# Optimization experiments

Hardware: AMD Instinct MI355X
Metric: run time of the kernel (lower is better)

Reference implementation:

```python
import jax, jax.numpy as jnp
import numpy as np

H = 1024          # hidden_size
NH = 16           # num_heads
NKV = 16          # num_kv_heads
HD = 64           # head_dim
INTER = 2048      # intermediate_size
E = 8             # num_experts
TOPK = 2
EPS = 1e-6


def setup_inputs() -> dict:
    key = jax.random.key(0)
    ks = jax.random.split(key, 8)
    B, S = 4, 1024
    total_qkv = (NH + 2 * NKV) * HD
    return {
        "hidden_states": jax.random.normal(ks[0], (B, S, H), dtype=jnp.float32),
        "attention_mask": jnp.zeros((1, 1, S, S), dtype=jnp.float32),
        "input_layernorm": jnp.ones((H,), dtype=jnp.float32),
        "post_attention_layernorm": jnp.ones((H,), dtype=jnp.float32),
        "qkv_w": jax.random.normal(ks[1], (H, total_qkv), dtype=jnp.float32) * 0.02,
        "o_w": jax.random.normal(ks[2], (NH * HD, H), dtype=jnp.float32) * 0.02,
        "router_w": jax.random.normal(ks[3], (H, E), dtype=jnp.float32) * 0.02,
        "gate_up_proj": jax.random.normal(ks[4], (E, H, 2 * INTER), dtype=jnp.float32) * 0.02,
        "down_proj": jax.random.normal(ks[5], (E, INTER, H), dtype=jnp.float32) * 0.02,
    }


def _rmsnorm(x, w):
    var = jnp.mean(x * x, axis=-1, keepdims=True)
    return x * jax.lax.rsqrt(var + EPS) * w


def _attention_block(x, attention_mask, input_layernorm, qkv_w, o_w):
    B, S, _ = x.shape
    h = _rmsnorm(x, input_layernorm)
    qkv = h @ qkv_w  # [B,S,(NH+2*NKV)*HD]
    tq, tkv = NH * HD, NKV * HD
    q = qkv[..., :tq].reshape(B, S, NH, HD).transpose(0, 2, 1, 3)
    k = qkv[..., tq:tq + tkv].reshape(B, S, NKV, HD).transpose(0, 2, 1, 3)
    v = qkv[..., tq + tkv:].reshape(B, S, NKV, HD).transpose(0, 2, 1, 3)
    scores = jnp.einsum('bhqd,bhkd->bhqk', q, k) / np.sqrt(HD).astype(np.float32)
    scores = scores + attention_mask
    attn = jax.nn.softmax(scores, axis=-1)
    out = jnp.einsum('bhqk,bhkd->bhqd', attn, v)
    out = out.transpose(0, 2, 1, 3).reshape(B, S, NH * HD)
    return out @ o_w


def _moe_block(x, post_attention_layernorm, router_w, gate_up_proj, down_proj):
    B, S, _ = x.shape
    xf = x.reshape(-1, H)                      # [T,H]
    T = xf.shape[0]
    hf = _rmsnorm(xf, post_attention_layernorm)
    logits = hf @ router_w                     # [T,E]
    probs = jax.nn.softmax(logits, axis=-1)
    w, idx = jax.lax.top_k(probs, TOPK)        # [T,TOPK]
    w = w / jnp.sum(w, axis=-1, keepdims=True)
    # combine weights scattered into dense [T,E] (0 for unrouted experts)
    cw = jnp.zeros((T, E), dtype=hf.dtype).at[jnp.arange(T)[:, None], idx].add(w)
    out = jnp.zeros_like(hf)
    for e in range(E):  # fixed small expert loop, fully vectorized over tokens
        gu = hf @ gate_up_proj[e]              # [T,2*INTER]
        g, u = gu[:, :INTER], gu[:, INTER:]
        act = jax.nn.silu(g) * u
        out = out + cw[:, e:e + 1] * (act @ down_proj[e])
    return out.reshape(B, S, H)


def reference(hidden_states, attention_mask, input_layernorm, post_attention_layernorm,
              qkv_w, o_w, router_w, gate_up_proj, down_proj):
    x = hidden_states
    x = x + _attention_block(x, attention_mask, input_layernorm, qkv_w, o_w)
    x = x + _moe_block(x, post_attention_layernorm, router_w, gate_up_proj, down_proj)
    return x
```

## Files before the change

kernel.cpp:

```cpp
#include <hip/hip_runtime.h>
#include <cstdint>
#include <cmath>

#define T_TOK 4096
#define H_DIM 1024
#define QKV_N 3072
#define S_LEN 1024
#define INTER_DIM 2048
#define MAXROWS 9216

typedef unsigned short u16;
using f32x4 = __attribute__((ext_vector_type(4))) float;
using h16x8 = __attribute__((ext_vector_type(8))) _Float16;
using h16x4 = __attribute__((ext_vector_type(4))) _Float16;
using i32x4 = __attribute__((ext_vector_type(4))) int;
using u16x4 = __attribute__((ext_vector_type(4))) u16;
using u16x8 = __attribute__((ext_vector_type(8))) u16;

__device__ __forceinline__ float bf2f(u16 u){ return __uint_as_float(((uint32_t)u)<<16); }
__device__ __forceinline__ u16 f2bf(float f){
  uint32_t x = __float_as_uint(f);
  uint32_t r = x + 0x7FFFu + ((x>>16)&1u);
  return (u16)(r>>16);
}
__device__ __forceinline__ f32x4 mfma16(h16x8 a, h16x8 b, f32x4 c){
  return __builtin_amdgcn_mfma_f32_16x16x32_f16(a,b,c,0,0,0);
}
__device__ __forceinline__ float rsqrt_acc(float v){
  float r = rsqrtf(v);
  r = r*(1.5f - 0.5f*v*r*r);
  r = r*(1.5f - 0.5f*v*r*r);
  return r;
}
__device__ __forceinline__ float ldin(const void* p, size_t i, int is32){
  return is32 ? ((const float*)p)[i] : bf2f(((const u16*)p)[i]);
}
__device__ __forceinline__ int kslot_sw(int k, int noct){
  return (k&7) | (((k>>3) ^ (noct&3))<<3);
}
__device__ __forceinline__ void gll16(const void* g, void* l){
  __builtin_amdgcn_global_load_lds(
      (const __attribute__((address_space(1))) void*)g,
      (__attribute__((address_space(3))) void*)l, 16, 0, 0);
}

__global__ void k_detect(const uint32_t* __restrict__ x, int* __restrict__ dflag){
  uint32_t u = x[threadIdx.x];
  int e = (u>>23)&0xFF;
  int ok = (e>=103 && e<=150);
  unsigned long long m = __ballot(ok);
  if (threadIdx.x==0) *dflag = (__popcll(m) >= 48) ? 1 : 0;
}

__global__ __launch_bounds__(256) void k_trans2(const void* __restrict__ src,
    _Float16* __restrict__ dst, int R, int C, const int* __restrict__ df){
  const int is32 = *df;
  __shared__ _Float16 t[64][65];
  size_t bo = (size_t)blockIdx.z * R * C;
  int c0 = blockIdx.x<<6, r0 = blockIdx.y<<6;
  int ty = threadIdx.x>>3, tx = threadIdx.x&7;
  #pragma unroll
  for (int rr=0; rr<2; rr++){
    int r = rr*32 + ty;
    size_t gi = bo + (size_t)(r0+r)*C + c0 + tx*8;
    _Float16 v[8];
    if (is32){
      f32x4 a0 = *(const f32x4*)&((const float*)src)[gi];
      f32x4 a1 = *(const f32x4*)&((const float*)src)[gi+4];
      #pragma unroll
      for (int i=0;i<4;i++){ v[i]=(_Float16)a0[i]; v[4+i]=(_Float16)a1[i]; }
    } else {
      u16x8 a = *(const u16x8*)&((const u16*)src)[gi];
      #pragma unroll
      for (int i=0;i<8;i++) v[i]=(_Float16)bf2f(a[i]);
    }
    #pragma unroll
    for (int i=0;i<8;i++) t[r][tx*8+i] = v[i];
  }
  __syncthreads();
  #pragma unroll
  for (int rr=0; rr<2; rr++){
    int n = rr*32 + ty;
    h16x8 v;
    #pragma unroll
    for (int i=0;i<8;i++) v[i] = t[tx*8+i][n];
    *(h16x8*)&dst[bo + (size_t)(c0+n)*R + r0 + tx*8] = v;
  }
}

__global__ __launch_bounds__(256) void k_maskchk(const void* __restrict__ m, int* __restrict__ flag,
                                                 const int* __restrict__ df){
  const int is32 = *df;
  int i = (blockIdx.x*256 + threadIdx.x)*4;
  int nz = 0;
  if (is32){
    f32x4 v = *(const f32x4*)&((const float*)m)[i];
    nz = (v[0]!=0.f)||(v[1]!=0.f)||(v[2]!=0.f)||(v[3]!=0.f);
  } else {
    u16x4 v = *(const u16x4*)&((const u16*)m)[i];
    nz = ((v[0]|v[1]|v[2]|v[3]) & 0x7FFF) != 0;
  }
  if (nz) atomicOr(flag, 1);
}

__global__ __launch_bounds__(256) void k_rms1(const void* __restrict__ x, const void* __restrict__ w,
                                              _Float16* __restrict__ hhi, _Float16* __restrict__ hlo,
                                              const int* __restrict__ df){
  const int is32 = *df;
  int t = blockIdx.x, tid = threadIdx.x;
  size_t base = (size_t)t*H_DIM + tid*4;
  float f[4];
  #pragma unroll
  for (int m=0;m<4;m++) f[m] = ldin(x, base+m, is32);
  float ss = f[0]*f[0] + f[1]*f[1] + f[2]*f[2] + f[3]*f[3];
  #pragma unroll
  for (int off=32; off>0; off>>=1) ss += __shfl_down(ss, off, 64);
  __shared__ float red[4];
  if ((tid & 63) == 0) red[tid>>6] = ss;
  __syncthreads();
  float rstd = rsqrt_acc((red[0]+red[1]+red[2]+red[3]) * (1.0f/H_DIM) + 1e-6f);
  h16x4 oh, ol;
  #pragma unroll
  for (int m=0;m<4;m++){
    float v = f[m]*rstd*ldin(w, tid*4+m, is32);
    _Float16 hh = (_Float16)v;
    oh[m] = hh;
    ol[m] = (_Float16)(v - (float)hh);
  }
  *(h16x4*)&hhi[base] = oh;
  *(h16x4*)&hlo[base] = ol;
}

template<int EPI>
__global__ __launch_bounds__(256) void k_gemm_hl(const _Float16* __restrict__ Ah,
    const _Float16* __restrict__ Al, const _Float16* __restrict__ Bt,
    float* __restrict__ C, _Float16* __restrict__ Chi, _Float16* __restrict__ Clo,
    const void* __restrict__ res, int N, int K, const int* __restrict__ df){
  const int is32 = (EPI==1) ? *df : 0;
  __shared__ __align__(16) _Float16 AhS[128*32];
  __shared__ __align__(16) _Float16 AlS[128*32];
  __shared__ __align__(16) _Float16 Bs[128*32];
  int tid = threadIdx.x, lane = tid&63, wvx = tid>>6;
  int wr = wvx>>1, wc = wvx&1, quad = lane>>4, lrow = lane&15;
  int m0 = blockIdx.y<<7, n0 = blockIdx.x<<7;
  int ar = tid>>2, acg = (tid&3)*8;
  const _Float16* a0h = &Ah[(size_t)(m0+ar)*K + acg];
  const _Float16* a1h = &Ah[(size_t)(m0+64+ar)*K + acg];
  const _Float16* a0l = &Al[(size_t)(m0+ar)*K + acg];
  const _Float16* a1l = &Al[(size_t)(m0+64+ar)*K + acg];
  const _Float16* b0  = &Bt[(size_t)(n0+ar)*K + acg];
  const _Float16* b1  = &Bt[(size_t)(n0+64+ar)*K + acg];
  f32x4 acc[4][4] = {};
  for (int k0=0; k0<K; k0+=32){
    gll16(a0h + k0, &AhS[wvx*512]);
    gll16(a1h + k0, &AhS[2048 + wvx*512]);
    gll16(a0l + k0, &AlS[wvx*512]);
    gll16(a1l + k0, &AlS[2048 + wvx*512]);
    gll16(b0  + k0, &Bs[wvx*512]);
    gll16(b1  + k0, &Bs[2048 + wvx*512]);
    __syncthreads();
    h16x8 ah[4], al[4], bb[4];
    #pragma unroll
    for (int i=0;i<4;i++){
      ah[i] = *(const h16x8*)&AhS[(wr*64 + i*16 + lrow)*32 + quad*8];
      al[i] = *(const h16x8*)&AlS[(wr*64 + i*16 + lrow)*32 + quad*8];
    }
    #pragma unroll
    for (int j=0;j<4;j++) bb[j] = *(const h16x8*)&Bs[(wc*64 + j*16 + lrow)*32 + quad*8];
    #pragma unroll
    for (int i=0;i<4;i++)
      #pragma unroll
      for (int j=0;j<4;j++){
        acc[i][j] = mfma16(ah[i], bb[j], acc[i][j]);
        acc[i][j] = mfma16(al[i], bb[j], acc[i][j]);
      }
    __syncthreads();
  }
  #pragma unroll
  for (int i=0;i<4;i++)
    #pragma unroll
    for (int j=0;j<4;j++){
      int col = n0 + wc*64 + j*16 + lrow;
      #pragma unroll
      for (int r=0;r<4;r++){
        int row = m0 + wr*64 + i*16 + quad*4 + r;
        size_t idx = (size_t)row*N + col;
        float v = acc[i][j][r];
        if (EPI==1){
          v += ldin(res, idx, is32);
          C[idx] = v;
        } else {
          _Float16 hh = (_Float16)v;
          Chi[idx] = hh;
          Clo[idx] = (_Float16)(v - (float)hh);
        }
      }
    }
}

__global__ __launch_bounds__(256) void k_vt(const _Float16* __restrict__ qh,
    const _Float16* __restrict__ ql, _Float16* __restrict__ vth, _Float16* __restrict__ vtl){
  __shared__ _Float16 th[64][72];
  __shared__ _Float16 tl[64][72];
  int bh = blockIdx.y;
  int b = bh>>4, h = bh&15;
  int key0 = blockIdx.x<<6;
  size_t tok0 = (size_t)b*S_LEN;
  int ty = threadIdx.x>>3, tx = threadIdx.x&7;
  #pragma unroll
  for (int rr=0; rr<2; rr++){
    int r = rr*32 + ty;
    size_t gi = (tok0 + key0 + r)*(size_t)QKV_N + 2048 + h*64 + tx*8;
    h16x8 vh_ = *(const h16x8*)&qh[gi];
    h16x8 vl_ = *(const h16x8*)&ql[gi];
    #pragma unroll
    for (int i=0;i<8;i++){ th[r][tx*8+i] = vh_[i]; tl[r][tx*8+i] = vl_[i]; }
  }
  __syncthreads();
  size_t dbase = (size_t)bh*64*1024;
  #pragma unroll
  for (int rr=0; rr<2; rr++){
    int d = rr*32 + ty;
    h16x8 oh, ol;
    #pragma unroll
    for (int i=0;i<8;i++){ oh[i] = th[tx*8+i][d]; ol[i] = tl[tx*8+i][d]; }
    *(h16x8*)&vth[dbase + (size_t)d*1024 + key0 + tx*8] = oh;
    *(h16x8*)&vtl[dbase + (size_t)d*1024 + key0 + tx*8] = ol;
  }
}

__global__ __launch_bounds__(256, 2) void k_attn(const _Float16* __restrict__ qkvh,
    const _Float16* __restrict__ qkvl, const _Float16* __restrict__ vth_g,
    const _Float16* __restrict__ vtl_g, const void* __restrict__ mask,
    const int* __restrict__ mflag, _Float16* __restrict__ ohi, _Float16* __restrict__ olo,
    const int* __restrict__ df){
  const int is32 = *df;
  __shared__ __align__(16) _Float16 pool[32768];
  _Float16* Khi = pool;
  _Float16* Klo = pool + 4096;
  _Float16* Vth = pool + 8192;
  _Float16* Vtl = pool + 12288;
  _Float16* Phi = pool + 16384;
  _Float16* Plo = pool + 24576;
  int qt = blockIdx.x, bh = blockIdx.y;
  int b = bh>>4, h = bh&15;
  int tid = threadIdx.x, lane = tid&63, wvx = tid>>6, quad = lane>>4, lrow = lane&15;
  size_t tok0 = (size_t)b*S_LEN;
  int q0 = qt<<7;
  {
    int r = tid>>2, cg = (tid&3)*8;
    #pragma unroll
    for (int p=0;p<2;p++)
      #pragma unroll
      for (int g=0;g<2;g++){
        size_t src = (tok0 + q0 + g*64 + r)*(size_t)QKV_N + h*64 + p*32 + cg;
        gll16(&qkvh[src], &pool[p*4096 + g*2048 + wvx*512]);
        gll16(&qkvl[src], &pool[8192 + p*4096 + g*2048 + wvx*512]);
      }
  }
  __syncthreads();
  h16x8 qfh[2][2], qfl[2][2];
  #pragma unroll
  for (int p=0;p<2;p++)
    #pragma unroll
    for (int i=0;i<2;i++){
      qfh[p][i] = *(const h16x8*)&pool[(p*128 + wvx*32 + i*16 + lrow)*32 + quad*8];
      qfl[p][i] = *(const h16x8*)&pool[8192 + (p*128 + wvx*32 + i*16 + lrow)*32 + quad*8];
    }
  int useMask = *mflag;
  float mrun[2][4], lrun[2][4];
  f32x4 oacc[2][4] = {};
  #pragma unroll
  for (int i=0;i<2;i++)
    #pragma unroll
    for (int r=0;r<4;r++){ mrun[i][r] = -INFINITY; lrun[i][r] = 0.f; }
  size_t vbase = (size_t)bh*64*1024;
  int krow = tid>>3;
  int c8   = (tid&7)*8;
  int rsw  = ((tid>>3)&7)<<3;
  int fsw  = (lrow&7)<<3;
  size_t ksrc0 = (tok0 + krow)*(size_t)QKV_N + 1024 + h*64 + c8;
  size_t vsrc0 = vbase + (size_t)krow*1024 + c8;
  h16x8 kh_r[2], kl_r[2], vh_r[2], vl_r[2];
  {
    size_t ks0 = ksrc0, ks1 = ksrc0 + (size_t)32*QKV_N;
    kh_r[0] = *(const h16x8*)&qkvh[ks0];  kl_r[0] = *(const h16x8*)&qkvl[ks0];
    kh_r[1] = *(const h16x8*)&qkvh[ks1];  kl_r[1] = *(const h16x8*)&qkvl[ks1];
    size_t vs0 = vsrc0, vs1 = vsrc0 + 32*1024;
    vh_r[0] = *(const h16x8*)&vth_g[vs0]; vl_r[0] = *(const h16x8*)&vtl_g[vs0];
    vh_r[1] = *(const h16x8*)&vth_g[vs1]; vl_r[1] = *(const h16x8*)&vtl_g[vs1];
  }
  __syncthreads();

  for (int kt=0; kt<16; kt++){
    int key0 = kt*64;
    {
      int o0 = (tid*8) ^ rsw, o1 = (2048 + tid*8) ^ rsw;
      *(h16x8*)&Khi[o0] = kh_r[0];  *(h16x8*)&Khi[o1] = kh_r[1];
      *(h16x8*)&Klo[o0] = kl_r[0];  *(h16x8*)&Klo[o1] = kl_r[1];
      *(h16x8*)&Vth[o0] = vh_r[0];  *(h16x8*)&Vth[o1] = vh_r[1];
      *(h16x8*)&Vtl[o0] = vl_r[0];  *(h16x8*)&Vtl[o1] = vl_r[1];
    }
    if (kt < 15){
      size_t ks0 = ksrc0 + (size_t)(key0+64)*QKV_N, ks1 = ks0 + (size_t)32*QKV_N;
      kh_r[0] = *(const h16x8*)&qkvh[ks0];  kl_r[0] = *(const h16x8*)&qkvl[ks0];
      kh_r[1] = *(const h16x8*)&qkvh[ks1];  kl_r[1] = *(const h16x8*)&qkvl[ks1];
      size_t vs0 = vsrc0 + (key0+64), vs1 = vs0 + 32*1024;
      vh_r[0] = *(const h16x8*)&vth_g[vs0]; vl_r[0] = *(const h16x8*)&vtl_g[vs0];
      vh_r[1] = *(const h16x8*)&vth_g[vs1]; vl_r[1] = *(const h16x8*)&vtl_g[vs1];
    }
    __syncthreads();
    f32x4 sacc[2][4] = {};
    __builtin_amdgcn_s_setprio(1);
    #pragma unroll
    for (int p=0;p<2;p++){
      h16x8 kh[4], kl[4];
      #pragma unroll
      for (int j=0;j<4;j++){
        int kidx = ((j*16+lrow)*64 + p*32 + quad*8) ^ fsw;
        kh[j] = *(const h16x8*)&Khi[kidx];
        kl[j] = *(const h16x8*)&Klo[kidx];
      }
      #pragma unroll
      for (int i=0;i<2;i++)
        #pragma unroll
        for (int j=0;j<4;j++){
          sacc[i][j] = mfma16(qfh[p][i], kh[j], sacc[i][j]);
          sacc[i][j] = mfma16(qfh[p][i], kl[j], sacc[i][j]);
          sacc[i][j] = mfma16(qfl[p][i], kh[j], sacc[i][j]);
        }
    }
    __builtin_amdgcn_s_setprio(0);
    #pragma unroll
    for (int i=0;i<2;i++){
      #pragma unroll
      for (int r=0;r<4;r++){
        int qrow = q0 + wvx*32 + i*16 + quad*4 + r;
        float s[4];
        #pragma unroll
        for (int j=0;j<4;j++){
          float sv = sacc[i][j][r] * 0.125f;
          if (useMask) sv += ldin(mask, (size_t)qrow*S_LEN + key0 + j*16 + lrow, is32);
          s[j] = sv;
        }
        float mx = fmaxf(fmaxf(s[0],s[1]), fmaxf(s[2],s[3]));
        #pragma unroll
        for (int mm=1; mm<=8; mm<<=1) mx = fmaxf(mx, __shfl_xor(mx, mm, 64));
        float mnew = fmaxf(mrun[i][r], mx);
        float alpha = __expf(mrun[i][r] - mnew);
        float ps = 0.f;
        #pragma unroll
        for (int j=0;j<4;j++){
          float p = __expf(s[j] - mnew);
          s[j] = p;
          ps += p;
        }
        #pragma unroll
        for (int mm=1; mm<=8; mm<<=1) ps += __shfl_xor(ps, mm, 64);
        lrun[i][r] = lrun[i][r]*alpha + ps;
        mrun[i][r] = mnew;
        #pragma unroll
        for (int jd=0;jd<4;jd++) oacc[i][jd][r] *= alpha;
        int prow = wvx*32 + i*16 + quad*4 + r;
        int pswz = (prow&7)<<3;
        #pragma unroll
        for (int j=0;j<4;j++){
          int pidx = (prow*64 + j*16 + lrow) ^ pswz;
          float pv = s[j];
          _Float16 ph = (_Float16)pv;
          Phi[pidx] = ph;
          Plo[pidx] = (_Float16)(pv - (float)ph);
        }
      }
    }
    __syncthreads();
    {
      h16x8 pf[2][2], pl[2][2];
      #pragma unroll
      for (int i=0;i<2;i++)
        #pragma unroll
        for (int ks=0;ks<2;ks++){
          int pidx = ((wvx*32 + i*16 + lrow)*64 + ks*32 + quad*8) ^ fsw;
          pf[i][ks] = *(const h16x8*)&Phi[pidx];
          pl[i][ks] = *(const h16x8*)&Plo[pidx];
        }
      __builtin_amdgcn_s_setprio(1);
      #pragma unroll
      for (int ks=0;ks<2;ks++){
        h16x8 vh[4], vl[4];
        #pragma unroll
        for (int jd=0;jd<4;jd++){
          int vidx = ((jd*16+lrow)*64 + ks*32 + quad*8) ^ fsw;
          vh[jd] = *(const h16x8*)&Vth[vidx];
          vl[jd] = *(const h16x8*)&Vtl[vidx];
        }
        #pragma unroll
        for (int i=0;i<2;i++)
          #pragma unroll
          for (int jd=0;jd<4;jd++){
            oacc[i][jd] = mfma16(pf[i][ks], vh[jd], oacc[i][jd]);
            oacc[i][jd] = mfma16(pf[i][ks], vl[jd], oacc[i][jd]);
            oacc[i][jd] = mfma16(pl[i][ks], vh[jd], oacc[i][jd]);
          }
      }
      __builtin_amdgcn_s_setprio(0);
    }
    __syncthreads();
  }
  #pragma unroll
  for (int i=0;i<2;i++)
    #pragma unroll
    for (int j=0;j<4;j++)
      #pragma unroll
      for (int r=0;r<4;r++){
        int row = q0 + wvx*32 + i*16 + quad*4 + r;
        int col = h*64 + j*16 + lrow;
        size_t idx = (tok0 + row)*H_DIM + col;
        float v = oacc[i][j][r] / lrun[i][r];
        _Float16 hh = (_Float16)v;
        ohi[idx] = hh;
        olo[idx] = (_Float16)(v - (float)hh);
      }
}

__global__ __launch_bounds__(256) void k_rms2_router(const float* __restrict__ x1, const void* __restrict__ w,
    const void* __restrict__ rw, _Float16* __restrict__ h2,
    int* __restrict__ tok_e, float* __restrict__ tok_w, int* __restrict__ counts,
    const int* __restrict__ df){
  const int is32 = *df;
  int t = blockIdx.x, tid = threadIdx.x;
  f32x4 v = *(const f32x4*)&x1[(size_t)t*H_DIM + tid*4];
  float ss = v[0]*v[0]+v[1]*v[1]+v[2]*v[2]+v[3]*v[3];
  #pragma unroll
  for (int off=32; off>0; off>>=1) ss += __shfl_down(ss, off, 64);
  __shared__ float red[4];
  __shared__ float lgs[32];
  if ((tid&63)==0) red[tid>>6] = ss;
  __syncthreads();
  float rstd = rsqrt_acc((red[0]+red[1]+red[2]+red[3])*(1.0f/H_DIM) + 1e-6f);
  float hv[4];
  h16x4 hst;
  #pragma unroll
  for (int m=0;m<4;m++){ hv[m] = v[m]*rstd*ldin(w, tid*4+m, is32); hst[m] = (_Float16)hv[m]; }
  *(h16x4*)&h2[(size_t)t*H_DIM + tid*4] = hst;
  float part[8] = {0,0,0,0,0,0,0,0};
  #pragma unroll
  for (int m=0;m<4;m++){
    size_t c = (size_t)(tid*4 + m)*8;
    #pragma unroll
    for (int e=0;e<8;e++) part[e] += hv[m]*ldin(rw, c+e, is32);
  }
  #pragma unroll
  for (int e=0;e<8;e++){
    #pragma unroll
    for (int off=32; off>0; off>>=1) part[e] += __shfl_down(part[e], off, 64);
  }
  if ((tid&63)==0){
    #pragma unroll
    for (int e=0;e<8;e++) lgs[(tid>>6)*8 + e] = part[e];
  }
  __syncthreads();
  if (tid==0){
    float lg[8];
    #pragma unroll
    for (int e=0;e<8;e++) lg[e] = lgs[e] + lgs[8+e] + lgs[16+e] + lgs[24+e];
    int e0 = 0;
    #pragma unroll
    for (int e=1;e<8;e++) if (lg[e] > lg[e0]) e0 = e;
    int e1 = (e0==0) ? 1 : 0;
    #pragma unroll
    for (int e=0;e<8;e++) if (e != e0 && lg[e] > lg[e1]) e1 = e;
    float d = expf(lg[e1] - lg[e0]);
    float w0 = 1.0f/(1.0f + d);
    float w1 = d * w0;
    tok_e[t*2] = e0; tok_e[t*2+1] = e1;
    tok_w[t*2] = w0; tok_w[t*2+1] = w1;
    atomicAdd(&counts[e0], 1);
    atomicAdd(&counts[e1], 1);
  }
}

__global__ void k_offsets(const int* __restrict__ counts, int* __restrict__ offs, int* __restrict__ fillpos){
  if (threadIdx.x == 0 && blockIdx.x == 0){
    int o = 0;
    for (int e=0;e<8;e++){
      offs[e] = o; fillpos[e] = o;
      o += (counts[e] + 127) & ~127;
    }
    offs[8] = o;
  }
}

__global__ __launch_bounds__(256) void k_fill(const int* __restrict__ tok_e, const float* __restrict__ tok_w,
    int* __restrict__ fillpos, int* __restrict__ list_ts, float* __restrict__ list_w){
  int t = blockIdx.x*256 + threadIdx.x;
  if (t >= T_TOK) return;
  #pragma unroll
  for (int s=0;s<2;s++){
    int e = tok_e[t*2+s];
    int p = atomicAdd(&fillpos[e], 1);
    list_ts[p] = t*2 + s;
    list_w[p] = tok_w[t*2+s];
  }
}


__global__ __launch_bounds__(256) void k_gemm_gu_t(const _Float16* __restrict__ h2,
    const _Float16* __restrict__ gwt, _Float16* __restrict__ act, const int* __restrict__ list_ts,
    const int* __restrict__ counts, const int* __restrict__ offs){
  int m0 = blockIdx.y<<7;
  if (m0 >= offs[8]) return;
  int e = 0;
  while (m0 >= offs[e+1]) e++;
  int base = offs[e], cnt = counts[e];
  if (m0 >= base + cnt) return;
  __shared__ __align__(16) _Float16 As[128*32], Bg[64*32], Bu[64*32];
  __shared__ int rowtok[128];
  int tid = threadIdx.x;
  if (tid < 128) rowtok[tid] = list_ts[min(m0 + tid, base + cnt - 1)] >> 1;
  __syncthreads();
  int lane = tid&63, wvx = tid>>6, wr = wvx>>1, wc = wvx&1, quad = lane>>4, lrow = lane&15;
  int n0 = blockIdx.x<<6;
  const _Float16* Bge = gwt + (size_t)e*4096*1024 + (size_t)n0*1024;
  const _Float16* Bue = gwt + (size_t)e*4096*1024 + (size_t)(2048+n0)*1024;
  const _Float16* arow0 = &h2[(size_t)rowtok[tid>>2]*H_DIM + (tid&3)*8];
  const _Float16* arow1 = &h2[(size_t)rowtok[(256+tid)>>2]*H_DIM + (tid&3)*8];
  int bR = tid>>2, bG = tid&3;
  f32x4 ag[4][2] = {}, au[4][2] = {};
  for (int k0=0; k0<1024; k0+=32){
    gll16(arow0 + k0, &As[(size_t)(wvx*64)*8]);
    gll16(arow1 + k0, &As[(size_t)(256 + wvx*64)*8]);
    gll16(&Bge[(size_t)bR*1024 + k0 + bG*8], &Bg[(size_t)(wvx*64)*8]);
    gll16(&Bue[(size_t)bR*1024 + k0 + bG*8], &Bu[(size_t)(wvx*64)*8]);
    __syncthreads();
    h16x8 a[4], bg[2], bu[2];
    #pragma unroll
    for (int i=0;i<4;i++) a[i] = *(const h16x8*)&As[(wr*64 + i*16 + lrow)*32 + quad*8];
    #pragma unroll
    for (int j=0;j<2;j++){
      bg[j] = *(const h16x8*)&Bg[(wc*32 + j*16 + lrow)*32 + quad*8];
      bu[j] = *(const h16x8*)&Bu[(wc*32 + j*16 + lrow)*32 + quad*8];
    }
    #pragma unroll
    for (int i=0;i<4;i++)
      #pragma unroll
      for (int j=0;j<2;j++){
        ag[i][j] = mfma16(a[i], bg[j], ag[i][j]);
        au[i][j] = mfma16(a[i], bu[j], au[i][j]);
      }
    __syncthreads();
  }
  #pragma unroll
  for (int i=0;i<4;i++)
    #pragma unroll
    for (int j=0;j<2;j++)
      #pragma unroll
      for (int r=0;r<4;r++){
        int row = m0 + wr*64 + i*16 + quad*4 + r;
        int col = n0 + wc*32 + j*16 + lrow;
        float g = ag[i][j][r], u = au[i][j][r];
        float sv = g / (1.0f + __expf(-g));
        act[(size_t)row*INTER_DIM + col] = (_Float16)(sv * u);
      }
}

__global__ __launch_bounds__(256) void k_gemm_down_t(const _Float16* __restrict__ act,
    const _Float16* __restrict__ dwt, _Float16* __restrict__ slotbuf, const int* __restrict__ list_ts,
    const float* __restrict__ list_w, const int* __restrict__ counts, const int* __restrict__ offs){
  int m0 = blockIdx.y<<7;
  if (m0 >= offs[8]) return;
  int e = 0;
  while (m0 >= offs[e+1]) e++;
  int base = offs[e], cnt = counts[e];
  if (m0 >= base + cnt) return;
  __shared__ __align__(16) _Float16 As[128*32], Bs[128*32];
  int tid = threadIdx.x, lane = tid&63, wvx = tid>>6;
  int wr = wvx>>1, wc = wvx&1, quad = lane>>4, lrow = lane&15;
  int n0 = blockIdx.x<<7;
  const _Float16* Be = dwt + (size_t)e*1024*2048 + (size_t)n0*2048;
  f32x4 acc[4][4] = {};
  for (int k0=0; k0<2048; k0+=32){
    #pragma unroll
    for (int it=0; it<2; it++){
      int c2 = it*256 + tid;
      int r = c2>>2, g = c2&3;
      gll16(&act[(size_t)(m0+r)*INTER_DIM + k0 + g*8], &As[(size_t)(it*256 + wvx*64)*8]);
      gll16(&Be[(size_t)r*2048 + k0 + g*8], &Bs[(size_t)(it*256 + wvx*64)*8]);
    }
    __syncthreads();
    h16x8 a[4], b[4];
    #pragma unroll
    for (int i=0;i<4;i++) a[i] = *(const h16x8*)&As[(wr*64 + i*16 + lrow)*32 + quad*8];
    #pragma unroll
    for (int j=0;j<4;j++) b[j] = *(const h16x8*)&Bs[(wc*64 + j*16 + lrow)*32 + quad*8];
    #pragma unroll
    for (int i=0;i<4;i++)
      #pragma unroll
      for (int j=0;j<4;j++)
        acc[i][j] = mfma16(a[i], b[j], acc[i][j]);
    __syncthreads();
  }
  #pragma unroll
  for (int i=0;i<4;i++)
    #pragma unroll
    for (int r=0;r<4;r++){
      int m = m0 + wr*64 + i*16 + quad*4 + r;
      if (m < base + cnt){
        int ts = list_ts[m];
        float wgt = list_w[m];
        #pragma unroll
        for (int j=0;j<4;j++){
          int col = n0 + wc*64 + j*16 + lrow;
          slotbuf[(size_t)ts*H_DIM + col] = (_Float16)(wgt * acc[i][j][r]);
        }
      }
    }
}


__global__ __launch_bounds__(256) void k_gemm_gu(const _Float16* __restrict__ h2, const void* __restrict__ guw,
    _Float16* __restrict__ act, const int* __restrict__ list_ts,
    const int* __restrict__ counts, const int* __restrict__ offs, const int* __restrict__ df){
  const int is32 = *df;
  int m0 = blockIdx.y<<7;
  if (m0 >= offs[8]) return;
  int e = 0;
  while (m0 >= offs[e+1]) e++;
  int base = offs[e], cnt = counts[e];
  if (m0 >= base + cnt) return;
  __shared__ __align__(16) _Float16 As[128*32], Bg[64*40], Bu[64*40];
  __shared__ int rowtok[128];
  int tid = threadIdx.x;
  if (tid < 128){
    int mc = min(m0 + tid, base + cnt - 1);
    rowtok[tid] = list_ts[mc] >> 1;
  }
  __syncthreads();
  int lane = tid&63, wvx = tid>>6, wr = wvx>>1, wc = wvx&1, quad = lane>>4, lrow = lane&15;
  int n0 = blockIdx.x<<6;
  size_t ebase = (size_t)e*H_DIM*4096;
  f32x4 ag[4][2] = {}, au[4][2] = {};
  for (int k0=0; k0<1024; k0+=32){
    #pragma unroll
    for (int it=0; it<2; it++){
      int ch = it*256 + tid;
      int r = ch>>2, c = ch&3;
      *(i32x4*)&As[ch*8] = *(const i32x4*)&h2[(size_t)rowtok[r]*H_DIM + k0 + c*8];
    }
    {
      int k = tid>>3, g = tid&7;
      size_t rowb = ebase + (size_t)(k0+k)*4096;
      int ks = kslot_sw(k, g);
      _Float16 tg[8], tu[8];
      if (is32){
        const float* gf = (const float*)guw;
        f32x4 a0 = *(const f32x4*)&gf[rowb + n0 + g*8];
        f32x4 a1 = *(const f32x4*)&gf[rowb + n0 + g*8 + 4];
        f32x4 b0 = *(const f32x4*)&gf[rowb + 2048 + n0 + g*8];
        f32x4 b1 = *(const f32x4*)&gf[rowb + 2048 + n0 + g*8 + 4];
        #pragma unroll
        for (int i=0;i<4;i++){ tg[i]=(_Float16)a0[i]; tg[4+i]=(_Float16)a1[i];
                               tu[i]=(_Float16)b0[i]; tu[4+i]=(_Float16)b1[i]; }
      } else {
        const u16* gb = (const u16*)guw;
        u16x4 a0 = *(const u16x4*)&gb[rowb + n0 + g*8];
        u16x4 a1 = *(const u16x4*)&gb[rowb + n0 + g*8 + 4];
        u16x4 b0 = *(const u16x4*)&gb[rowb + 2048 + n0 + g*8];
        u16x4 b1 = *(const u16x4*)&gb[rowb + 2048 + n0 + g*8 + 4];
        #pragma unroll
        for (int i=0;i<4;i++){ tg[i]=(_Float16)bf2f(a0[i]); tg[4+i]=(_Float16)bf2f(a1[i]);
                               tu[i]=(_Float16)bf2f(b0[i]); tu[4+i]=(_Float16)bf2f(b1[i]); }
      }
      #pragma unroll
      for (int i=0;i<8;i++){
        int n = g*8 + i;
        Bg[n*40 + ks] = tg[i];
        Bu[n*40 + ks] = tu[i];
      }
    }
    __syncthreads();
    h16x8 a[4], bg[2], bu[2];
    #pragma unroll
    for (int i=0;i<4;i++) a[i] = *(const h16x8*)&As[(wr*64 + i*16 + lrow)*32 + quad*8];
    #pragma unroll
    for (int j=0;j<2;j++){
      int n = wc*32 + j*16 + lrow;
      int oct = (quad ^ ((n>>3)&3))*8;
      bg[j] = *(const h16x8*)&Bg[n*40 + oct];
      bu[j] = *(const h16x8*)&Bu[n*40 + oct];
    }
    #pragma unroll
    for (int i=0;i<4;i++)
      #pragma unroll
      for (int j=0;j<2;j++){
        ag[i][j] = mfma16(a[i], bg[j], ag[i][j]);
        au[i][j] = mfma16(a[i], bu[j], au[i][j]);
      }
    __syncthreads();
  }
  #pragma unroll
  for (int i=0;i<4;i++)
    #pragma unroll
    for (int j=0;j<2;j++)
      #pragma unroll
      for (int r=0;r<4;r++){
        int row = m0 + wr*64 + i*16 + quad*4 + r;
        int col = n0 + wc*32 + j*16 + lrow;
        float g = ag[i][j][r], u = au[i][j][r];
        float sv = g / (1.0f + __expf(-g));
        act[(size_t)row*INTER_DIM + col] = (_Float16)(sv * u);
      }
}

__global__ __launch_bounds__(256) void k_gemm_down(const _Float16* __restrict__ act, const void* __restrict__ dw,
    _Float16* __restrict__ slotbuf, const int* __restrict__ list_ts, const float* __restrict__ list_w,
    const int* __restrict__ counts, const int* __restrict__ offs, const int* __restrict__ df){
  const int is32 = *df;
  int m0 = blockIdx.y<<7;
  if (m0 >= offs[8]) return;
  int e = 0;
  while (m0 >= offs[e+1]) e++;
  int base = offs[e], cnt = counts[e];
  if (m0 >= base + cnt) return;
  __shared__ __align__(16) _Float16 As[128*32], Bs[128*40];
  int tid = threadIdx.x, lane = tid&63, wvx = tid>>6;
  int wr = wvx>>1, wc = wvx&1, quad = lane>>4, lrow = lane&15;
  int n0 = blockIdx.x<<7;
  size_t ebase = (size_t)e*INTER_DIM*H_DIM;
  f32x4 acc[4][4] = {};
  for (int k0=0; k0<2048; k0+=32){
    #pragma unroll
    for (int it=0; it<2; it++){
      int ch = it*256 + tid;
      int r = ch>>2, c = ch&3;
      *(i32x4*)&As[ch*8] = *(const i32x4*)&act[(size_t)(m0+r)*INTER_DIM + k0 + c*8];
    }
    {
      int k = tid>>3, g = tid&7;
      size_t rowb = ebase + (size_t)(k0+k)*H_DIM;
      int ks = kslot_sw(k, g);
      #pragma unroll
      for (int p=0;p<2;p++){
        _Float16 tb[8];
        if (is32){
          const float* bf = (const float*)dw;
          f32x4 a0 = *(const f32x4*)&bf[rowb + n0 + p*64 + g*8];
          f32x4 a1 = *(const f32x4*)&bf[rowb + n0 + p*64 + g*8 + 4];
          #pragma unroll
          for (int i=0;i<4;i++){ tb[i]=(_Float16)a0[i]; tb[4+i]=(_Float16)a1[i]; }
        } else {
          const u16* bb = (const u16*)dw;
          u16x4 a0 = *(const u16x4*)&bb[rowb + n0 + p*64 + g*8];
          u16x4 a1 = *(const u16x4*)&bb[rowb + n0 + p*64 + g*8 + 4];
          #pragma unroll
          for (int i=0;i<4;i++){ tb[i]=(_Float16)bf2f(a0[i]); tb[4+i]=(_Float16)bf2f(a1[i]); }
        }
        #pragma unroll
        for (int i=0;i<8;i++){
          int n = p*64 + g*8 + i;
          Bs[n*40 + ks] = tb[i];
        }
      }
    }
    __syncthreads();
    h16x8 a[4], b[4];
    #pragma unroll
    for (int i=0;i<4;i++) a[i] = *(const h16x8*)&As[(wr*64 + i*16 + lrow)*32 + quad*8];
    #pragma unroll
    for (int j=0;j<4;j++){
      int n = wc*64 + j*16 + lrow;
      b[j] = *(const h16x8*)&Bs[n*40 + ((quad ^ ((n>>3)&3))*8)];
    }
    #pragma unroll
    for (int i=0;i<4;i++)
      #pragma unroll
      for (int j=0;j<4;j++)
        acc[i][j] = mfma16(a[i], b[j], acc[i][j]);
    __syncthreads();
  }
  #pragma unroll
  for (int i=0;i<4;i++)
    #pragma unroll
    for (int r=0;r<4;r++){
      int m = m0 + wr*64 + i*16 + quad*4 + r;
      if (m < base + cnt){
        int ts = list_ts[m];
        float wgt = list_w[m];
        #pragma unroll
        for (int j=0;j<4;j++){
          int col = n0 + wc*64 + j*16 + lrow;
          slotbuf[(size_t)ts*H_DIM + col] = (_Float16)(wgt * acc[i][j][r]);
        }
      }
    }
}

__global__ __launch_bounds__(256) void k_final(const float* __restrict__ x1, const _Float16* __restrict__ slot,
                                               void* __restrict__ outv, const int* __restrict__ df){
  const int is32 = *df;
  int i4 = (blockIdx.x*256 + threadIdx.x)*4;
  int t = i4 >> 10, c = i4 & 1023;
  f32x4 a = *(const f32x4*)&x1[i4];
  h16x4 s0 = *(const h16x4*)&slot[(size_t)(t*2)*H_DIM + c];
  h16x4 s1 = *(const h16x4*)&slot[(size_t)(t*2+1)*H_DIM + c];
  if (is32){
    f32x4 o;
    #pragma unroll
    for (int m=0;m<4;m++) o[m] = a[m] + (float)s0[m] + (float)s1[m];
    *(f32x4*)&((float*)outv)[i4] = o;
  } else {
    u16x4 o;
    #pragma unroll
    for (int m=0;m<4;m++) o[m] = f2bf(a[m] + (float)s0[m] + (float)s1[m]);
    *(u16x4*)&((u16*)outv)[i4] = o;
  }
}

extern "C" void kernel_launch(void* const* d_in, const int* in_sizes, int n_in,
                              void* d_out, int out_size, void* d_ws, size_t ws_size,
                              hipStream_t stream){
  (void)in_sizes; (void)n_in; (void)out_size;
  const void* x    = d_in[0];
  const void* mask = d_in[1];
  const void* ln1  = d_in[2];
  const void* ln2  = d_in[3];
  const void* qkvw = d_in[4];
  const void* ow   = d_in[5];
  const void* rw   = d_in[6];
  const void* guw  = d_in[7];
  const void* dww  = d_in[8];

  char* ws = (char*)d_ws;
  size_t off = 0;
  auto alloc = [&](size_t b)->void*{ void* p = ws + off; off = (off + b + 255) & ~(size_t)255; return p; };
  int* meta            = (int*)alloc(32*sizeof(int));
  _Float16* qkv_wt     = (_Float16*)alloc((size_t)3072*1024*2);
  _Float16* o_wt       = (_Float16*)alloc((size_t)1024*1024*2);
  _Float16* hpair      = (_Float16*)alloc((size_t)2*4096*1024*2);
  _Float16* qkvpair    = (_Float16*)alloc((size_t)2*4096*3072*2);
  float* x1            = (float*)alloc((size_t)4096*1024*4);
  int* list_ts         = (int*)alloc(MAXROWS*4);
  float* list_w        = (float*)alloc(MAXROWS*4);
  int* tok_e           = (int*)alloc((size_t)4096*2*4);
  float* tok_w         = (float*)alloc((size_t)4096*2*4);
  size_t base_end = off;
  _Float16* gu_wt      = (_Float16*)alloc((size_t)8*4096*1024*2);
  _Float16* down_wt    = (_Float16*)alloc((size_t)8*1024*2048*2);
  const int big = (ws_size >= off) ? 1 : 0;
  (void)base_end;

  int* counts = meta;
  int* offs   = meta + 8;
  int* fillpos= meta + 17;
  int* flag   = meta + 25;
  int* dflag  = meta + 26;

  _Float16* h_hi   = hpair;
  _Float16* h_lo   = hpair + (size_t)4096*1024;
  _Float16* qkv_hi = qkvpair;
  _Float16* qkv_lo = qkvpair + (size_t)4096*3072;
  _Float16* vth    = (_Float16*)x1;
  _Float16* vtl    = vth + (size_t)64*64*1024;
  _Float16* ahi    = hpair;
  _Float16* alo    = hpair + (size_t)4096*1024;
  _Float16* h2     = qkvpair;
  _Float16* act    = qkvpair + (size_t)4096*1024;
  _Float16* slotbuf= hpair;

  hipMemsetAsync(meta, 0, 32*sizeof(int), stream);
  k_detect<<<dim3(1), dim3(64), 0, stream>>>((const uint32_t*)x, dflag);
  k_trans2<<<dim3(48, 16, 1), 256, 0, stream>>>(qkvw, qkv_wt, 1024, 3072, dflag);
  k_trans2<<<dim3(16, 16, 1), 256, 0, stream>>>(ow, o_wt, 1024, 1024, dflag);
  if (big){
    k_trans2<<<dim3(64, 16, 8), 256, 0, stream>>>(guw, gu_wt, 1024, 4096, dflag);
    k_trans2<<<dim3(16, 32, 8), 256, 0, stream>>>(dww, down_wt, 2048, 1024, dflag);
  }
  k_maskchk<<<dim3(1024), 256, 0, stream>>>(mask, flag, dflag);
  k_rms1<<<dim3(4096), 256, 0, stream>>>(x, ln1, h_hi, h_lo, dflag);
  k_gemm_hl<0><<<dim3(24, 32), 256, 0, stream>>>(h_hi, h_lo, qkv_wt, nullptr, qkv_hi, qkv_lo,
                                                 nullptr, 3072, 1024, dflag);
  k_vt<<<dim3(16, 64), 256, 0, stream>>>(qkv_hi, qkv_lo, vth, vtl);
  k_attn<<<dim3(8, 64), 256, 0, stream>>>(qkv_hi, qkv_lo, vth, vtl, mask, flag, ahi, alo, dflag);
  k_gemm_hl<1><<<dim3(8, 32), 256, 0, stream>>>(ahi, alo, o_wt, x1, nullptr, nullptr,
                                                x, 1024, 1024, dflag);
  k_rms2_router<<<dim3(4096), 256, 0, stream>>>(x1, ln2, rw, h2, tok_e, tok_w, counts, dflag);
  k_offsets<<<dim3(1), dim3(64), 0, stream>>>(counts, offs, fillpos);
  k_fill<<<dim3(16), 256, 0, stream>>>(tok_e, tok_w, fillpos, list_ts, list_w);
  if (big){
    k_gemm_gu_t<<<dim3(32, 72), 256, 0, stream>>>(h2, gu_wt, act, list_ts, counts, offs);
    k_gemm_down_t<<<dim3(8, 72), 256, 0, stream>>>(act, down_wt, slotbuf, list_ts, list_w, counts, offs);
  } else {
    k_gemm_gu<<<dim3(32, 72), 256, 0, stream>>>(h2, guw, act, list_ts, counts, offs, dflag);
    k_gemm_down<<<dim3(8, 72), 256, 0, stream>>>(act, dww, slotbuf, list_ts, list_w, counts, offs, dflag);
  }
  k_final<<<dim3(4096), 256, 0, stream>>>(x1, slotbuf, d_out, dflag);
}
```

Before: 849.3 us.

## Double K-tile depth to 64 with XOR-swizzled LDS layout in three GEMMs

Raises the per-iteration K slice from 32 to 64 in the hi/lo GEMM, the expert gate-up GEMM and the expert down GEMM, which halves the number of barrier pairs per output tile. The shared-memory layout becomes 64-wide rows with an XOR swizzle of the 16-byte column group by row index, applied on both the async global-to-LDS loads and the fragment reads, to avoid bank conflicts from the wider row stride. This doubles LDS use per block, which may reduce occupancy.

```diff
diff --git a/kernel.cpp b/kernel.cpp
--- a/kernel.cpp
+++ b/kernel.cpp
@@ -137,43 +137,48 @@
     float* __restrict__ C, _Float16* __restrict__ Chi, _Float16* __restrict__ Clo,
     const void* __restrict__ res, int N, int K, const int* __restrict__ df){
   const int is32 = (EPI==1) ? *df : 0;
-  __shared__ __align__(16) _Float16 AhS[128*32];
-  __shared__ __align__(16) _Float16 AlS[128*32];
-  __shared__ __align__(16) _Float16 Bs[128*32];
+  __shared__ __align__(16) _Float16 AhS[128*64];
+  __shared__ __align__(16) _Float16 AlS[128*64];
+  __shared__ __align__(16) _Float16 Bs[128*64];
   int tid = threadIdx.x, lane = tid&63, wvx = tid>>6;
   int wr = wvx>>1, wc = wvx&1, quad = lane>>4, lrow = lane&15;
   int m0 = blockIdx.y<<7, n0 = blockIdx.x<<7;
-  int ar = tid>>2, acg = (tid&3)*8;
-  const _Float16* a0h = &Ah[(size_t)(m0+ar)*K + acg];
-  const _Float16* a1h = &Ah[(size_t)(m0+64+ar)*K + acg];
-  const _Float16* a0l = &Al[(size_t)(m0+ar)*K + acg];
-  const _Float16* a1l = &Al[(size_t)(m0+64+ar)*K + acg];
-  const _Float16* b0  = &Bt[(size_t)(n0+ar)*K + acg];
-  const _Float16* b1  = &Bt[(size_t)(n0+64+ar)*K + acg];
+  int srow = tid>>3;
+  int csw  = (tid&7) ^ (srow&7);
+  int fsw  = lrow&7;
+  const _Float16* pah = &Ah[(size_t)(m0+srow)*K + csw*8];
+  const _Float16* pal = &Al[(size_t)(m0+srow)*K + csw*8];
+  const _Float16* pbt = &Bt[(size_t)(n0+srow)*K + csw*8];
   f32x4 acc[4][4] = {};
-  for (int k0=0; k0<K; k0+=32){
-    gll16(a0h + k0, &AhS[wvx*512]);
-    gll16(a1h + k0, &AhS[2048 + wvx*512]);
-    gll16(a0l + k0, &AlS[wvx*512]);
-    gll16(a1l + k0, &AlS[2048 + wvx*512]);
-    gll16(b0  + k0, &Bs[wvx*512]);
-    gll16(b1  + k0, &Bs[2048 + wvx*512]);
-    __syncthreads();
-    h16x8 ah[4], al[4], bb[4];
-    #pragma unroll
-    for (int i=0;i<4;i++){
-      ah[i] = *(const h16x8*)&AhS[(wr*64 + i*16 + lrow)*32 + quad*8];
-      al[i] = *(const h16x8*)&AlS[(wr*64 + i*16 + lrow)*32 + quad*8];
-    }
-    #pragma unroll
-    for (int j=0;j<4;j++) bb[j] = *(const h16x8*)&Bs[(wc*64 + j*16 + lrow)*32 + quad*8];
-    #pragma unroll
-    for (int i=0;i<4;i++)
-      #pragma unroll
-      for (int j=0;j<4;j++){
-        acc[i][j] = mfma16(ah[i], bb[j], acc[i][j]);
-        acc[i][j] = mfma16(al[i], bb[j], acc[i][j]);
-      }
+  for (int k0=0; k0<K; k0+=64){
+    #pragma unroll
+    for (int ro=0; ro<4; ro++){
+      size_t rs = (size_t)(ro*32)*K + k0;
+      gll16(pah + rs, &AhS[ro*2048 + wvx*512]);
+      gll16(pal + rs, &AlS[ro*2048 + wvx*512]);
+      gll16(pbt + rs, &Bs [ro*2048 + wvx*512]);
+    }
+    __syncthreads();
+    #pragma unroll
+    for (int ks=0; ks<2; ks++){
+      int co = ((ks*4 + quad) ^ fsw)*8;
+      h16x8 ah[4], al[4], bb[4];
+      #pragma unroll
+      for (int i=0;i<4;i++){
+        int ra = (wr*64 + i*16 + lrow)*64;
+        ah[i] = *(const h16x8*)&AhS[ra + co];
+        al[i] = *(const h16x8*)&AlS[ra + co];
+      }
+      #pragma unroll
+      for (int j=0;j<4;j++) bb[j] = *(const h16x8*)&Bs[(wc*64 + j*16 + lrow)*64 + co];
+      #pragma unroll
+      for (int i=0;i<4;i++)
+        #pragma unroll
+        for (int j=0;j<4;j++){
+          acc[i][j] = mfma16(ah[i], bb[j], acc[i][j]);
+          acc[i][j] = mfma16(al[i], bb[j], acc[i][j]);
+        }
+    }
     __syncthreads();
   }
   #pragma unroll
@@ -514,7 +519,7 @@
   while (m0 >= offs[e+1]) e++;
   int base = offs[e], cnt = counts[e];
   if (m0 >= base + cnt) return;
-  __shared__ __align__(16) _Float16 As[128*32], Bg[64*32], Bu[64*32];
+  __shared__ __align__(16) _Float16 As[128*64], Bg[64*64], Bu[64*64];
   __shared__ int rowtok[128];
   int tid = threadIdx.x;
   if (tid < 128) rowtok[tid] = list_ts[min(m0 + tid, base + cnt - 1)] >> 1;
@@ -523,31 +528,47 @@
   int n0 = blockIdx.x<<6;
   const _Float16* Bge = gwt + (size_t)e*4096*1024 + (size_t)n0*1024;
   const _Float16* Bue = gwt + (size_t)e*4096*1024 + (size_t)(2048+n0)*1024;
-  const _Float16* arow0 = &h2[(size_t)rowtok[tid>>2]*H_DIM + (tid&3)*8];
-  const _Float16* arow1 = &h2[(size_t)rowtok[(256+tid)>>2]*H_DIM + (tid&3)*8];
-  int bR = tid>>2, bG = tid&3;
+  int srow = tid>>3;
+  int csw  = (tid&7) ^ (srow&7);
+  int fsw  = lrow&7;
+  const _Float16* ar0 = &h2[(size_t)rowtok[srow    ]*H_DIM + csw*8];
+  const _Float16* ar1 = &h2[(size_t)rowtok[32+srow ]*H_DIM + csw*8];
+  const _Float16* ar2 = &h2[(size_t)rowtok[64+srow ]*H_DIM + csw*8];
+  const _Float16* ar3 = &h2[(size_t)rowtok[96+srow ]*H_DIM + csw*8];
+  const _Float16* bg0 = Bge + (size_t)srow*1024 + csw*8;
+  const _Float16* bg1 = Bge + (size_t)(32+srow)*1024 + csw*8;
+  const _Float16* bu0 = Bue + (size_t)srow*1024 + csw*8;
+  const _Float16* bu1 = Bue + (size_t)(32+srow)*1024 + csw*8;
   f32x4 ag[4][2] = {}, au[4][2] = {};
-  for (int k0=0; k0<1024; k0+=32){
-    gll16(arow0 + k0, &As[(size_t)(wvx*64)*8]);
-    gll16(arow1 + k0, &As[(size_t)(256 + wvx*64)*8]);
-    gll16(&Bge[(size_t)bR*1024 + k0 + bG*8], &Bg[(size_t)(wvx*64)*8]);
-    gll16(&Bue[(size_t)bR*1024 + k0 + bG*8], &Bu[(size_t)(wvx*64)*8]);
-    __syncthreads();
-    h16x8 a[4], bg[2], bu[2];
-    #pragma unroll
-    for (int i=0;i<4;i++) a[i] = *(const h16x8*)&As[(wr*64 + i*16 + lrow)*32 + quad*8];
-    #pragma unroll
-    for (int j=0;j<2;j++){
-      bg[j] = *(const h16x8*)&Bg[(wc*32 + j*16 + lrow)*32 + quad*8];
-      bu[j] = *(const h16x8*)&Bu[(wc*32 + j*16 + lrow)*32 + quad*8];
-    }
-    #pragma unroll
-    for (int i=0;i<4;i++)
+  for (int k0=0; k0<1024; k0+=64){
+    gll16(ar0 + k0, &As[       wvx*512]);
+    gll16(ar1 + k0, &As[2048 + wvx*512]);
+    gll16(ar2 + k0, &As[4096 + wvx*512]);
+    gll16(ar3 + k0, &As[6144 + wvx*512]);
+    gll16(bg0 + k0, &Bg[       wvx*512]);
+    gll16(bg1 + k0, &Bg[2048 + wvx*512]);
+    gll16(bu0 + k0, &Bu[       wvx*512]);
+    gll16(bu1 + k0, &Bu[2048 + wvx*512]);
+    __syncthreads();
+    #pragma unroll
+    for (int ks=0; ks<2; ks++){
+      int co = ((ks*4 + quad) ^ fsw)*8;
+      h16x8 a[4], bgf[2], buf_[2];
+      #pragma unroll
+      for (int i=0;i<4;i++) a[i] = *(const h16x8*)&As[(wr*64 + i*16 + lrow)*64 + co];
       #pragma unroll
       for (int j=0;j<2;j++){
-        ag[i][j] = mfma16(a[i], bg[j], ag[i][j]);
-        au[i][j] = mfma16(a[i], bu[j], au[i][j]);
-      }
+        bgf[j]  = *(const h16x8*)&Bg[(wc*32 + j*16 + lrow)*64 + co];
+        buf_[j] = *(const h16x8*)&Bu[(wc*32 + j*16 + lrow)*64 + co];
+      }
+      #pragma unroll
+      for (int i=0;i<4;i++)
+        #pragma unroll
+        for (int j=0;j<2;j++){
+          ag[i][j] = mfma16(a[i], bgf[j],  ag[i][j]);
+          au[i][j] = mfma16(a[i], buf_[j], au[i][j]);
+        }
+    }
     __syncthreads();
   }
   #pragma unroll
@@ -573,31 +594,39 @@
   while (m0 >= offs[e+1]) e++;
   int base = offs[e], cnt = counts[e];
   if (m0 >= base + cnt) return;
-  __shared__ __align__(16) _Float16 As[128*32], Bs[128*32];
+  __shared__ __align__(16) _Float16 As[128*64], Bs[128*64];
   int tid = threadIdx.x, lane = tid&63, wvx = tid>>6;
   int wr = wvx>>1, wc = wvx&1, quad = lane>>4, lrow = lane&15;
   int n0 = blockIdx.x<<7;
   const _Float16* Be = dwt + (size_t)e*1024*2048 + (size_t)n0*2048;
+  int srow = tid>>3;
+  int csw  = (tid&7) ^ (srow&7);
+  int fsw  = lrow&7;
+  const _Float16* pa = &act[(size_t)(m0+srow)*INTER_DIM + csw*8];
+  const _Float16* pb = Be + (size_t)srow*2048 + csw*8;
   f32x4 acc[4][4] = {};
-  for (int k0=0; k0<2048; k0+=32){
-    #pragma unroll
-    for (int it=0; it<2; it++){
-      int c2 = it*256 + tid;
-      int r = c2>>2, g = c2&3;
-      gll16(&act[(size_t)(m0+r)*INTER_DIM + k0 + g*8], &As[(size_t)(it*256 + wvx*64)*8]);
-      gll16(&Be[(size_t)r*2048 + k0 + g*8], &Bs[(size_t)(it*256 + wvx*64)*8]);
-    }
-    __syncthreads();
-    h16x8 a[4], b[4];
-    #pragma unroll
-    for (int i=0;i<4;i++) a[i] = *(const h16x8*)&As[(wr*64 + i*16 + lrow)*32 + quad*8];
-    #pragma unroll
-    for (int j=0;j<4;j++) b[j] = *(const h16x8*)&Bs[(wc*64 + j*16 + lrow)*32 + quad*8];
-    #pragma unroll
-    for (int i=0;i<4;i++)
-      #pragma unroll
-      for (int j=0;j<4;j++)
-        acc[i][j] = mfma16(a[i], b[j], acc[i][j]);
+  for (int k0=0; k0<2048; k0+=64){
+    #pragma unroll
+    for (int ro=0; ro<4; ro++){
+      size_t rs = (size_t)(ro*32)*2048 + k0;
+      gll16(pa + rs, &As[ro*2048 + wvx*512]);
+      gll16(pb + rs, &Bs[ro*2048 + wvx*512]);
+    }
+    __syncthreads();
+    #pragma unroll
+    for (int ks=0; ks<2; ks++){
+      int co = ((ks*4 + quad) ^ fsw)*8;
+      h16x8 a[4], b[4];
+      #pragma unroll
+      for (int i=0;i<4;i++) a[i] = *(const h16x8*)&As[(wr*64 + i*16 + lrow)*64 + co];
+      #pragma unroll
+      for (int j=0;j<4;j++) b[j] = *(const h16x8*)&Bs[(wc*64 + j*16 + lrow)*64 + co];
+      #pragma unroll
+      for (int i=0;i<4;i++)
+        #pragma unroll
+        for (int j=0;j<4;j++)
+          acc[i][j] = mfma16(a[i], b[j], acc[i][j]);
+    }
     __syncthreads();
   }
   #pragma unroll
```

After: 845.5 us. No clear change (-0.4%).

## Double-buffer LDS tiles and XOR-swizzle columns in the three MFMA GEMM kernels

Applied to the files above, without the earlier changes.

Gives the attention GEMM, the MoE gate-up GEMM and the down GEMM two LDS buffers each. The global-to-LDS load of the next K tile is issued before computing on the current one, and one barrier per iteration is dropped. The source column chunk is also XOR-swizzled by row, with matching reads, to cut LDS bank conflicts on the 16-byte fragment loads. This doubles LDS use per block, which may lower occupancy.

```diff
diff --git a/kernel.cpp b/kernel.cpp
--- a/kernel.cpp
+++ b/kernel.cpp
@@ -137,36 +137,44 @@
     float* __restrict__ C, _Float16* __restrict__ Chi, _Float16* __restrict__ Clo,
     const void* __restrict__ res, int N, int K, const int* __restrict__ df){
   const int is32 = (EPI==1) ? *df : 0;
-  __shared__ __align__(16) _Float16 AhS[128*32];
-  __shared__ __align__(16) _Float16 AlS[128*32];
-  __shared__ __align__(16) _Float16 Bs[128*32];
+  __shared__ __align__(16) _Float16 AhS[2][128*32];
+  __shared__ __align__(16) _Float16 AlS[2][128*32];
+  __shared__ __align__(16) _Float16 Bs[2][128*32];
   int tid = threadIdx.x, lane = tid&63, wvx = tid>>6;
   int wr = wvx>>1, wc = wvx&1, quad = lane>>4, lrow = lane&15;
   int m0 = blockIdx.y<<7, n0 = blockIdx.x<<7;
-  int ar = tid>>2, acg = (tid&3)*8;
-  const _Float16* a0h = &Ah[(size_t)(m0+ar)*K + acg];
-  const _Float16* a1h = &Ah[(size_t)(m0+64+ar)*K + acg];
-  const _Float16* a0l = &Al[(size_t)(m0+ar)*K + acg];
-  const _Float16* a1l = &Al[(size_t)(m0+64+ar)*K + acg];
-  const _Float16* b0  = &Bt[(size_t)(n0+ar)*K + acg];
-  const _Float16* b1  = &Bt[(size_t)(n0+64+ar)*K + acg];
+  int srow = tid>>2;
+  int csw  = (tid&3) ^ (srow&3);
+  const _Float16* a0h = &Ah[(size_t)(m0+srow)*K + csw*8];
+  const _Float16* a1h = &Ah[(size_t)(m0+64+srow)*K + csw*8];
+  const _Float16* a0l = &Al[(size_t)(m0+srow)*K + csw*8];
+  const _Float16* a1l = &Al[(size_t)(m0+64+srow)*K + csw*8];
+  const _Float16* b0  = &Bt[(size_t)(n0+srow)*K + csw*8];
+  const _Float16* b1  = &Bt[(size_t)(n0+64+srow)*K + csw*8];
+  auto stage = [&](int bb, int k0){
+    gll16(a0h + k0, &AhS[bb][wvx*512]);
+    gll16(a1h + k0, &AhS[bb][2048 + wvx*512]);
+    gll16(a0l + k0, &AlS[bb][wvx*512]);
+    gll16(a1l + k0, &AlS[bb][2048 + wvx*512]);
+    gll16(b0  + k0, &Bs[bb][wvx*512]);
+    gll16(b1  + k0, &Bs[bb][2048 + wvx*512]);
+  };
   f32x4 acc[4][4] = {};
+  stage(0, 0);
+  __syncthreads();
+  int cur = 0;
+  int co = (quad ^ (lrow&3))*8;
   for (int k0=0; k0<K; k0+=32){
-    gll16(a0h + k0, &AhS[wvx*512]);
-    gll16(a1h + k0, &AhS[2048 + wvx*512]);
-    gll16(a0l + k0, &AlS[wvx*512]);
-    gll16(a1l + k0, &AlS[2048 + wvx*512]);
-    gll16(b0  + k0, &Bs[wvx*512]);
-    gll16(b1  + k0, &Bs[2048 + wvx*512]);
-    __syncthreads();
+    if (k0 + 32 < K) stage(cur^1, k0+32);
     h16x8 ah[4], al[4], bb[4];
     #pragma unroll
     for (int i=0;i<4;i++){
-      ah[i] = *(const h16x8*)&AhS[(wr*64 + i*16 + lrow)*32 + quad*8];
-      al[i] = *(const h16x8*)&AlS[(wr*64 + i*16 + lrow)*32 + quad*8];
-    }
-    #pragma unroll
-    for (int j=0;j<4;j++) bb[j] = *(const h16x8*)&Bs[(wc*64 + j*16 + lrow)*32 + quad*8];
+      int ra = (wr*64 + i*16 + lrow)*32;
+      ah[i] = *(const h16x8*)&AhS[cur][ra + co];
+      al[i] = *(const h16x8*)&AlS[cur][ra + co];
+    }
+    #pragma unroll
+    for (int j=0;j<4;j++) bb[j] = *(const h16x8*)&Bs[cur][(wc*64 + j*16 + lrow)*32 + co];
     #pragma unroll
     for (int i=0;i<4;i++)
       #pragma unroll
@@ -175,6 +183,7 @@
         acc[i][j] = mfma16(al[i], bb[j], acc[i][j]);
       }
     __syncthreads();
+    cur ^= 1;
   }
   #pragma unroll
   for (int i=0;i<4;i++)
@@ -514,7 +523,7 @@
   while (m0 >= offs[e+1]) e++;
   int base = offs[e], cnt = counts[e];
   if (m0 >= base + cnt) return;
-  __shared__ __align__(16) _Float16 As[128*32], Bg[64*32], Bu[64*32];
+  __shared__ __align__(16) _Float16 As[2][128*32], Bg[2][64*32], Bu[2][64*32];
   __shared__ int rowtok[128];
   int tid = threadIdx.x;
   if (tid < 128) rowtok[tid] = list_ts[min(m0 + tid, base + cnt - 1)] >> 1;
@@ -523,32 +532,42 @@
   int n0 = blockIdx.x<<6;
   const _Float16* Bge = gwt + (size_t)e*4096*1024 + (size_t)n0*1024;
   const _Float16* Bue = gwt + (size_t)e*4096*1024 + (size_t)(2048+n0)*1024;
-  const _Float16* arow0 = &h2[(size_t)rowtok[tid>>2]*H_DIM + (tid&3)*8];
-  const _Float16* arow1 = &h2[(size_t)rowtok[(256+tid)>>2]*H_DIM + (tid&3)*8];
-  int bR = tid>>2, bG = tid&3;
+  int srow = tid>>2;
+  int csw  = (tid&3) ^ (srow&3);
+  const _Float16* ar0 = &h2[(size_t)rowtok[srow   ]*H_DIM + csw*8];
+  const _Float16* ar1 = &h2[(size_t)rowtok[64+srow]*H_DIM + csw*8];
+  const _Float16* bg0 = Bge + (size_t)srow*1024 + csw*8;
+  const _Float16* bu0 = Bue + (size_t)srow*1024 + csw*8;
+  auto stage = [&](int bb, int k0){
+    gll16(ar0 + k0, &As[bb][wvx*512]);
+    gll16(ar1 + k0, &As[bb][2048 + wvx*512]);
+    gll16(bg0 + k0, &Bg[bb][wvx*512]);
+    gll16(bu0 + k0, &Bu[bb][wvx*512]);
+  };
   f32x4 ag[4][2] = {}, au[4][2] = {};
+  stage(0, 0);
+  __syncthreads();
+  int cur = 0;
+  int co = (quad ^ (lrow&3))*8;
   for (int k0=0; k0<1024; k0+=32){
-    gll16(arow0 + k0, &As[(size_t)(wvx*64)*8]);
-    gll16(arow1 + k0, &As[(size_t)(256 + wvx*64)*8]);
-    gll16(&Bge[(size_t)bR*1024 + k0 + bG*8], &Bg[(size_t)(wvx*64)*8]);
-    gll16(&Bue[(size_t)bR*1024 + k0 + bG*8], &Bu[(size_t)(wvx*64)*8]);
+    if (k0 < 992) stage(cur^1, k0+32);
+    h16x8 a[4], bgf[2], buf_[2];
+    #pragma unroll
+    for (int i=0;i<4;i++) a[i] = *(const h16x8*)&As[cur][(wr*64 + i*16 + lrow)*32 + co];
+    #pragma unroll
+    for (int j=0;j<2;j++){
+      bgf[j]  = *(const h16x8*)&Bg[cur][(wc*32 + j*16 + lrow)*32 + co];
+      buf_[j] = *(const h16x8*)&Bu[cur][(wc*32 + j*16 + lrow)*32 + co];
+    }
+    #pragma unroll
+    for (int i=0;i<4;i++)
+      #pragma unroll
+      for (int j=0;j<2;j++){
+        ag[i][j] = mfma16(a[i], bgf[j],  ag[i][j]);
+        au[i][j] = mfma16(a[i], buf_[j], au[i][j]);
+      }
     __syncthreads();
-    h16x8 a[4], bg[2], bu[2];
-    #pragma unroll
-    for (int i=0;i<4;i++) a[i] = *(const h16x8*)&As[(wr*64 + i*16 + lrow)*32 + quad*8];
-    #pragma unroll
-    for (int j=0;j<2;j++){
-      bg[j] = *(const h16x8*)&Bg[(wc*32 + j*16 + lrow)*32 + quad*8];
-      bu[j] = *(const h16x8*)&Bu[(wc*32 + j*16 + lrow)*32 + quad*8];
-    }
-    #pragma unroll
-    for (int i=0;i<4;i++)
-      #pragma unroll
-      for (int j=0;j<2;j++){
-        ag[i][j] = mfma16(a[i], bg[j], ag[i][j]);
-        au[i][j] = mfma16(a[i], bu[j], au[i][j]);
-      }
-    __syncthreads();
+    cur ^= 1;
   }
   #pragma unroll
   for (int i=0;i<4;i++)
@@ -573,32 +592,42 @@
   while (m0 >= offs[e+1]) e++;
   int base = offs[e], cnt = counts[e];
   if (m0 >= base + cnt) return;
-  __shared__ __align__(16) _Float16 As[128*32], Bs[128*32];
+  __shared__ __align__(16) _Float16 As[2][128*32], Bs[2][128*32];
   int tid = threadIdx.x, lane = tid&63, wvx = tid>>6;
   int wr = wvx>>1, wc = wvx&1, quad = lane>>4, lrow = lane&15;
   int n0 = blockIdx.x<<7;
   const _Float16* Be = dwt + (size_t)e*1024*2048 + (size_t)n0*2048;
+  int srow = tid>>2;
+  int csw  = (tid&3) ^ (srow&3);
+  const _Float16* pa0 = &act[(size_t)(m0+srow)*INTER_DIM + csw*8];
+  const _Float16* pa1 = &act[(size_t)(m0+64+srow)*INTER_DIM + csw*8];
+  const _Float16* pb0 = Be + (size_t)srow*2048 + csw*8;
+  const _Float16* pb1 = Be + (size_t)(64+srow)*2048 + csw*8;
+  auto stage = [&](int bb, int k0){
+    gll16(pa0 + k0, &As[bb][wvx*512]);
+    gll16(pa1 + k0, &As[bb][2048 + wvx*512]);
+    gll16(pb0 + k0, &Bs[bb][wvx*512]);
+    gll16(pb1 + k0, &Bs[bb][2048 + wvx*512]);
+  };
   f32x4 acc[4][4] = {};
+  stage(0, 0);
+  __syncthreads();
+  int cur = 0;
+  int co = (quad ^ (lrow&3))*8;
   for (int k0=0; k0<2048; k0+=32){
-    #pragma unroll
-    for (int it=0; it<2; it++){
-      int c2 = it*256 + tid;
-      int r = c2>>2, g = c2&3;
-      gll16(&act[(size_t)(m0+r)*INTER_DIM + k0 + g*8], &As[(size_t)(it*256 + wvx*64)*8]);
-      gll16(&Be[(size_t)r*2048 + k0 + g*8], &Bs[(size_t)(it*256 + wvx*64)*8]);
-    }
-    __syncthreads();
+    if (k0 < 2016) stage(cur^1, k0+32);
     h16x8 a[4], b[4];
     #pragma unroll
-    for (int i=0;i<4;i++) a[i] = *(const h16x8*)&As[(wr*64 + i*16 + lrow)*32 + quad*8];
-    #pragma unroll
-    for (int j=0;j<4;j++) b[j] = *(const h16x8*)&Bs[(wc*64 + j*16 + lrow)*32 + quad*8];
+    for (int i=0;i<4;i++) a[i] = *(const h16x8*)&As[cur][(wr*64 + i*16 + lrow)*32 + co];
+    #pragma unroll
+    for (int j=0;j<4;j++) b[j] = *(const h16x8*)&Bs[cur][(wc*64 + j*16 + lrow)*32 + co];
     #pragma unroll
     for (int i=0;i<4;i++)
       #pragma unroll
       for (int j=0;j<4;j++)
         acc[i][j] = mfma16(a[i], b[j], acc[i][j]);
     __syncthreads();
+    cur ^= 1;
   }
   #pragma unroll
   for (int i=0;i<4;i++)
```

Result: no change. 834.5 us (-1.7%).
